# Performance work log

Hardware: AMD Instinct MI355X
Metric: run time of the kernel (lower is better)

Reference implementation:

```python
import jax, jax.numpy as jnp
import numpy as np

INPUT_SIZE = 3072
CORE_SIZE = 1024
OUTPUT_SIZE = 100
BATCH = 8192


def _ri(key, shape, lo, hi):
    # small-range int8 values (torch rand*scale cast to int8)
    return jax.random.randint(key, shape, lo, hi, dtype=jnp.int32).astype(jnp.int8)


def setup_inputs() -> dict:
    key = jax.random.key(0)
    ks = jax.random.split(key, 14)
    return {
        # learned int8 weights (nonzero after EQI.apply updates)
        "W_itoc": _ri(ks[0], (INPUT_SIZE, CORE_SIZE), -3, 4),
        "W_itoc_b": _ri(ks[1], (CORE_SIZE,), -3, 4),
        "W_ctoc": _ri(ks[2], (CORE_SIZE, CORE_SIZE), -3, 4),
        "W_ctoc_b": _ri(ks[3], (CORE_SIZE,), -3, 4),
        "W_ctoo": _ri(ks[4], (CORE_SIZE, OUTPUT_SIZE), -3, 4),
        "W_ctoo_b": _ri(ks[5], (OUTPUT_SIZE,), -3, 4),
        # epsilon perturbations: EPSILON_SCALE=2 -> values in {-1,0,1}
        "e_itoc": _ri(ks[6], (INPUT_SIZE, CORE_SIZE), -2, 2),
        "e_itoc_b": _ri(ks[7], (CORE_SIZE,), -2, 2),
        "e_ctoc": _ri(ks[8], (CORE_SIZE, CORE_SIZE), -2, 2),
        "e_ctoc_b": _ri(ks[9], (CORE_SIZE,), -2, 2),
        "e_ctoo": _ri(ks[10], (CORE_SIZE, OUTPUT_SIZE), -2, 2),
        "e_ctoo_b": _ri(ks[11], (OUTPUT_SIZE,), -2, 2),
        # forward activations
        "inputs": _ri(ks[12], (BATCH, INPUT_SIZE), -4, 5),
        "hiddens": _ri(ks[13], (BATCH, CORE_SIZE), -4, 5),
    }


def _addmm_i8(x, w, b):
    # int8 addmm with wraparound semantics: accumulate in int32, cast back
    # to int8 (truncation == mod-256, matching torch int8 arithmetic).
    acc = jnp.matmul(x.astype(jnp.int32), w.astype(jnp.int32)) + b.astype(jnp.int32)
    return acc.astype(jnp.int8)


def reference(W_itoc, W_itoc_b, W_ctoc, W_ctoc_b, W_ctoo, W_ctoo_b,
              e_itoc, e_itoc_b, e_ctoc, e_ctoc_b, e_ctoo, e_ctoo_b,
              inputs, hiddens):
    # layer 1: inputs -> core (weight = W + epsilon, elementwise int8 add)
    i2c = _addmm_i8(inputs, W_itoc + e_itoc, W_itoc_b + e_itoc_b)      # [B, CORE]
    # layer 2: (hiddens + projected inputs) -> core
    h2 = _addmm_i8(hiddens + i2c, W_ctoc + e_ctoc, W_ctoc_b + e_ctoc_b)  # [B, CORE]
    # layer 3: core -> output
    out = _addmm_i8(h2, W_ctoo + e_ctoo, W_ctoo_b + e_ctoo_b)          # [B, OUT]
    return (h2, out)
```

## Files before the change

kernel.cpp:

```cpp
#include <hip/hip_runtime.h>

typedef int v4i  __attribute__((ext_vector_type(4)));
typedef int v16i __attribute__((ext_vector_type(16)));

__device__ __forceinline__ int pack4i(int a, int b, int c, int d) {
  return (a & 255) | ((b & 255) << 8) | ((c & 255) << 16) | ((d & 255) << 24);
}
__device__ __forceinline__ int badd4(int a, int b) {
  return ((a & 0x7f7f7f7f) + (b & 0x7f7f7f7f)) ^ ((a ^ b) & 0x80808080);
}

#define MFMA_I8(a, b, c) __builtin_amdgcn_mfma_i32_32x32x32_i8(a, b, c, 0, 0, 0)
#define WAITV(N) asm volatile("s_waitcnt vmcnt(" #N ")" ::: "memory")
#define BARX do { asm volatile("s_waitcnt lgkmcnt(0)" ::: "memory"); \
                  __builtin_amdgcn_s_barrier(); } while (0)

__device__ void pack_tile(const int* __restrict__ W, const int* __restrict__ E,
                          char* __restrict__ Bt, int K, int N,
                          int nx, int ky, char* lin) {
  const int t = threadIdx.x;
  const int n0 = nx * 64, k0 = ky * 256;
  {
    const int c  = t & 15;
    const int kq = t >> 4;
    const int ng = n0 + c * 4;
    #pragma unroll 4
    for (int s = 0; s < 16; ++s) {
      const int k = s * 16 + kq;
      const long grow = (long)(k0 + k) * N;
      int a0, a1, a2, a3;
      if (ng + 3 < N) {
        int4 wv = *(const int4*)(W + grow + ng);
        int4 ev = *(const int4*)(E + grow + ng);
        a0 = wv.x + ev.x; a1 = wv.y + ev.y; a2 = wv.z + ev.z; a3 = wv.w + ev.w;
      } else {
        a0 = (ng + 0 < N) ? W[grow + ng + 0] + E[grow + ng + 0] : 0;
        a1 = (ng + 1 < N) ? W[grow + ng + 1] + E[grow + ng + 1] : 0;
        a2 = (ng + 2 < N) ? W[grow + ng + 2] + E[grow + ng + 2] : 0;
        a3 = (ng + 3 < N) ? W[grow + ng + 3] + E[grow + ng + 3] : 0;
      }
      *(int*)(lin + k * 68 + c * 4) = pack4i(a0, a1, a2, a3);
    }
  }
  __syncthreads();
  {
    const int n = t & 63, kq = t >> 6;
    char* dst = Bt + (long)(n0 + n) * K + k0 + (kq << 6);
    int outv[16];
    #pragma unroll
    for (int g = 0; g < 16; ++g) {
      const int k = (kq << 6) + (g << 2);
      outv[g] = pack4i(lin[(k + 0) * 68 + n], lin[(k + 1) * 68 + n],
                       lin[(k + 2) * 68 + n], lin[(k + 3) * 68 + n]);
    }
    #pragma unroll
    for (int g = 0; g < 4; ++g)
      *(int4*)(dst + (g << 4)) =
          make_int4(outv[g * 4], outv[g * 4 + 1], outv[g * 4 + 2], outv[g * 4 + 3]);
  }
}

__global__ __launch_bounds__(256) void pack_weights_kernel(
    const int* W1, const int* E1, char* Bt1,
    const int* W2, const int* E2, char* Bt2,
    const int* W3, const int* E3, char* Bt3,
    const int* b1, const int* eb1, int* bs1,
    const int* b2, const int* eb2, int* bs2,
    const int* b3, const int* eb3, int* bs3) {
  __shared__ __align__(16) char smem[17408];
  const int bid = blockIdx.x;
  if (bid < 192) {
    pack_tile(W1, E1, Bt1, 3072, 1024, bid % 16, bid / 16, smem);
  } else if (bid < 256) {
    const int l = bid - 192;
    pack_tile(W2, E2, Bt2, 1024, 1024, l % 16, l / 16, smem);
  } else if (bid < 264) {
    const int l = bid - 256;
    pack_tile(W3, E3, Bt3, 1024, 100, l & 1, l >> 1, smem);
  } else {
    const int t = threadIdx.x;
    for (int i = t; i < 1024; i += 256) {
      bs1[i] = b1[i] + eb1[i];
      bs2[i] = b2[i] + eb2[i];
    }
    for (int i = t; i < 128; i += 256)
      bs3[i] = (i < 100) ? (b3[i] + eb3[i]) : 0;
  }
}

__global__ __launch_bounds__(256, 2) void gemm1_kernel(
    const int* __restrict__ X, const char* __restrict__ Btg,
    const int* __restrict__ bsum, const int* __restrict__ H,
    char* __restrict__ A8out) {
  constexpr int K = 3072, KIT = 48;
  __shared__ __align__(16) char smem[61440];
  const int t = threadIdx.x;
  const int bid = blockIdx.x;
  const int mt = bid & 63, nt = bid >> 6;
  const long m0 = (long)mt << 7;
  const int n0 = nt << 7;

  const int lane = t & 63, w = t >> 6;
  const int lc = lane & 31, hg = lane >> 5;
  const int wm = w >> 1, wn = w & 1;

  v16i acc[2][2] = {};

  const int ar = t >> 4, ac = t & 15;
  const int* Xbase = X + (m0 + ar) * (long)K + ac * 4;
  const int awo = ar * 80 + ac * 4;
  const int r = t >> 2, q = t & 3;
  const char* Br0 = Btg + (long)(n0 + r) * K + q * 16;
  const char* Br1 = Br0 + (long)64 * K;
  const int bwo = 10240 + r * 80 + q * 16;

  const int fa = (wm * 64 + lc) * 80;
  const int fb = 10240 + (wn * 64 + lc) * 80;

  int4 xA[8], yA[8], xB0, xB1, yB0, yB1;

  auto ISSUEX = [&](int kt) {
    const int ko = kt * 64;
    #pragma unroll
    for (int j = 0; j < 8; ++j)
      xA[j] = *(const int4*)(Xbase + (long)j * 16 * K + ko);
    xB0 = *(const int4*)(Br0 + ko);
    xB1 = *(const int4*)(Br1 + ko);
  };
  auto ISSUEY = [&](int kt) {
    const int ko = kt * 64;
    #pragma unroll
    for (int j = 0; j < 8; ++j)
      yA[j] = *(const int4*)(Xbase + (long)j * 16 * K + ko);
    yB0 = *(const int4*)(Br0 + ko);
    yB1 = *(const int4*)(Br1 + ko);
  };
  auto WRITEX = [&](int st) {
    char* base = smem + st * 20480;
    #pragma unroll
    for (int j = 0; j < 8; ++j)
      *(int*)(base + awo + j * 16 * 80) =
          pack4i(xA[j].x, xA[j].y, xA[j].z, xA[j].w);
    *(int4*)(base + bwo)           = xB0;
    *(int4*)(base + bwo + 64 * 80) = xB1;
  };
  auto WRITEY = [&](int st) {
    char* base = smem + st * 20480;
    #pragma unroll
    for (int j = 0; j < 8; ++j)
      *(int*)(base + awo + j * 16 * 80) =
          pack4i(yA[j].x, yA[j].y, yA[j].z, yA[j].w);
    *(int4*)(base + bwo)           = yB0;
    *(int4*)(base + bwo + 64 * 80) = yB1;
  };
  auto MSTEP = [&](int st) {
    const char* base = smem + st * 20480;
    __builtin_amdgcn_s_setprio(1);
    #pragma unroll
    for (int ks = 0; ks < 2; ++ks) {
      const int sel = ks * 32 + hg * 16;
      v4i a0 = *(const v4i*)(base + fa + sel);
      v4i a1 = *(const v4i*)(base + fa + 32 * 80 + sel);
      v4i b0 = *(const v4i*)(base + fb + sel);
      v4i b1 = *(const v4i*)(base + fb + 32 * 80 + sel);
      acc[0][0] = MFMA_I8(a0, b0, acc[0][0]);
      acc[0][1] = MFMA_I8(a0, b1, acc[0][1]);
      acc[1][0] = MFMA_I8(a1, b0, acc[1][0]);
      acc[1][1] = MFMA_I8(a1, b1, acc[1][1]);
    }
    __builtin_amdgcn_s_setprio(0);
  };

  ISSUEX(0);
  ISSUEY(1);
  WAITV(10);
  WRITEX(0);
  BARX;
  for (int kt = 0; kt < KIT - 2; kt += 2) {
    ISSUEX(kt + 2);
    MSTEP(kt % 3);
    WAITV(10);
    WRITEY((kt + 1) % 3);
    BARX;
    ISSUEY(kt + 3);
    MSTEP((kt + 1) % 3);
    WAITV(10);
    WRITEX((kt + 2) % 3);
    BARX;
  }
  MSTEP((KIT - 2) % 3);
  WAITV(0);
  WRITEY((KIT - 1) % 3);
  BARX;
  MSTEP((KIT - 1) % 3);

  BARX;
  const int bsv0 = bsum[n0 + wn * 64 + lc];
  const int bsv1 = bsum[n0 + wn * 64 + 32 + lc];
  #pragma unroll
  for (int i = 0; i < 2; ++i) {
    #pragma unroll
    for (int j = 0; j < 2; ++j) {
      const int bv = j ? bsv1 : bsv0;
      const int col = wn * 64 + j * 32 + lc;
      #pragma unroll
      for (int rr = 0; rr < 16; ++rr) {
        const int row = wm * 64 + i * 32 + (hg << 2) + (rr & 3) + ((rr >> 2) << 3);
        smem[row * 136 + col] = (char)(acc[i][j][rr] + bv);
      }
    }
  }
  BARX;
  const char* srcp = smem + (t >> 1) * 136 + (t & 1) * 64;
  const long gco = (m0 + (t >> 1)) * 1024 + n0 + (t & 1) * 64;
  const int* hp = H + gco;
  #pragma unroll
  for (int g = 0; g < 4; ++g) {
    int4 s  = *(const int4*)(srcp + g * 16);
    int4 h0 = *(const int4*)(hp + g * 16);
    int4 h1 = *(const int4*)(hp + g * 16 + 4);
    int4 h2 = *(const int4*)(hp + g * 16 + 8);
    int4 h3 = *(const int4*)(hp + g * 16 + 12);
    s = make_int4(badd4(s.x, pack4i(h0.x, h0.y, h0.z, h0.w)),
                  badd4(s.y, pack4i(h1.x, h1.y, h1.z, h1.w)),
                  badd4(s.z, pack4i(h2.x, h2.y, h2.z, h2.w)),
                  badd4(s.w, pack4i(h3.x, h3.y, h3.z, h3.w)));
    *(int4*)(A8out + gco + g * 16) = s;
  }
}

__global__ __launch_bounds__(256, 2) void gemm2_kernel(
    const char* __restrict__ A, const char* __restrict__ Btg,
    const int* __restrict__ bsum, int* __restrict__ Iout) {
  constexpr int K = 1024, KIT = 16;
  __shared__ __align__(16) char smem[61440];
  const int t = threadIdx.x;
  const int bid = blockIdx.x;
  const int mt = bid & 63, nt = bid >> 6;
  const long m0 = (long)mt << 7;
  const int n0 = nt << 7;

  const int lane = t & 63, w = t >> 6;
  const int lc = lane & 31, hg = lane >> 5;
  const int wm = w >> 1, wn = w & 1;

  v16i acc[2][2] = {};

  const int r = t >> 2, q = t & 3;
  const char* Ar0 = A + (m0 + r) * (long)K + q * 16;
  const char* Ar1 = Ar0 + (long)64 * K;
  const char* Br0 = Btg + (long)(n0 + r) * K + q * 16;
  const char* Br1 = Br0 + (long)64 * K;
  const int awo = r * 80 + q * 16;
  const int bwo = 10240 + r * 80 + q * 16;

  const int fa = (wm * 64 + lc) * 80;
  const int fb = 10240 + (wn * 64 + lc) * 80;

  int4 xA0, xA1, xB0, xB1, yA0, yA1, yB0, yB1;

  auto ISSUEX = [&](int kt) {
    const int ko = kt * 64;
    xA0 = *(const int4*)(Ar0 + ko);
    xA1 = *(const int4*)(Ar1 + ko);
    xB0 = *(const int4*)(Br0 + ko);
    xB1 = *(const int4*)(Br1 + ko);
  };
  auto ISSUEY = [&](int kt) {
    const int ko = kt * 64;
    yA0 = *(const int4*)(Ar0 + ko);
    yA1 = *(const int4*)(Ar1 + ko);
    yB0 = *(const int4*)(Br0 + ko);
    yB1 = *(const int4*)(Br1 + ko);
  };
  auto WRITEX = [&](int st) {
    char* base = smem + st * 20480;
    *(int4*)(base + awo)           = xA0;
    *(int4*)(base + awo + 64 * 80) = xA1;
    *(int4*)(base + bwo)           = xB0;
    *(int4*)(base + bwo + 64 * 80) = xB1;
  };
  auto WRITEY = [&](int st) {
    char* base = smem + st * 20480;
    *(int4*)(base + awo)           = yA0;
    *(int4*)(base + awo + 64 * 80) = yA1;
    *(int4*)(base + bwo)           = yB0;
    *(int4*)(base + bwo + 64 * 80) = yB1;
  };
  auto MSTEP = [&](int st) {
    const char* base = smem + st * 20480;
    __builtin_amdgcn_s_setprio(1);
    #pragma unroll
    for (int ks = 0; ks < 2; ++ks) {
      const int sel = ks * 32 + hg * 16;
      v4i a0 = *(const v4i*)(base + fa + sel);
      v4i a1 = *(const v4i*)(base + fa + 32 * 80 + sel);
      v4i b0 = *(const v4i*)(base + fb + sel);
      v4i b1 = *(const v4i*)(base + fb + 32 * 80 + sel);
      acc[0][0] = MFMA_I8(a0, b0, acc[0][0]);
      acc[0][1] = MFMA_I8(a0, b1, acc[0][1]);
      acc[1][0] = MFMA_I8(a1, b0, acc[1][0]);
      acc[1][1] = MFMA_I8(a1, b1, acc[1][1]);
    }
    __builtin_amdgcn_s_setprio(0);
  };

  ISSUEX(0);
  ISSUEY(1);
  WAITV(4);
  WRITEX(0);
  BARX;
  for (int kt = 0; kt < KIT - 2; kt += 2) {
    ISSUEX(kt + 2);
    MSTEP(kt % 3);
    WAITV(4);
    WRITEY((kt + 1) % 3);
    BARX;
    ISSUEY(kt + 3);
    MSTEP((kt + 1) % 3);
    WAITV(4);
    WRITEX((kt + 2) % 3);
    BARX;
  }
  MSTEP((KIT - 2) % 3);
  WAITV(0);
  WRITEY((KIT - 1) % 3);
  BARX;
  MSTEP((KIT - 1) % 3);

  const int bsj0 = bsum[n0 + wn * 64 + lc];
  const int bsj1 = bsum[n0 + wn * 64 + 32 + lc];
  #pragma unroll
  for (int i = 0; i < 2; ++i) {
    #pragma unroll
    for (int j = 0; j < 2; ++j) {
      const int bv = j ? bsj1 : bsj0;
      const int col = n0 + wn * 64 + j * 32 + lc;
      #pragma unroll
      for (int rr = 0; rr < 16; ++rr) {
        const long row = m0 + wm * 64 + i * 32 + (hg << 2) + (rr & 3) + ((rr >> 2) << 3);
        Iout[row * 1024 + col] = (int)(signed char)(acc[i][j][rr] + bv);
      }
    }
  }
}

__global__ __launch_bounds__(256, 2) void gemm3_kernel(
    const int* __restrict__ h2, const char* __restrict__ Btg,
    const int* __restrict__ bsum, int* __restrict__ Iout) {
  __shared__ __align__(16) char smem[23040];
  const int t = threadIdx.x;
  const int m0 = blockIdx.x << 4;
  const int lane = t & 63, w = t >> 6;
  const int l16 = lane & 15, q = lane >> 4;
  v4i acc0 = {}, acc1 = {};

  const int am = t >> 4, ah = t & 15;
  const int* Arow = h2 + (long)(m0 + am) * 1024 + ah * 4;
  const int aoff = am * 80 + ah * 4;
  const int bm = t >> 1, bh = t & 1;
  const char* Brow = Btg + (long)bm * 1024 + bh * 32;
  const int boff = bm * 80 + bh * 32;

  const int abo  = l16 * 80 + q * 16;
  const int bbo0 = (w * 32 + l16) * 80 + q * 16;
  const int bbo1 = (w * 32 + 16 + l16) * 80 + q * 16;

  int4 ar, br0, br1;
  auto LOAD = [&](int kt) {
    const int kb = kt << 6;
    ar  = *(const int4*)(Arow + kb);
    br0 = *(const int4*)(Brow + kb);
    br1 = *(const int4*)(Brow + kb + 16);
  };
  auto STORE = [&](int stage) {
    char* base = smem + stage * 11520;
    *(int*)(base + aoff) = pack4i(ar.x, ar.y, ar.z, ar.w);
    *(int4*)(base + 1280 + boff)      = br0;
    *(int4*)(base + 1280 + boff + 16) = br1;
  };
  auto MFMA = [&](int stage) {
    const char* base = smem + stage * 11520;
    v4i a  = *(const v4i*)(base + abo);
    v4i b0 = *(const v4i*)(base + 1280 + bbo0);
    v4i b1 = *(const v4i*)(base + 1280 + bbo1);
    acc0 = __builtin_amdgcn_mfma_i32_16x16x64_i8(a, b0, acc0, 0, 0, 0);
    acc1 = __builtin_amdgcn_mfma_i32_16x16x64_i8(a, b1, acc1, 0, 0, 0);
  };

  LOAD(0); STORE(0); __syncthreads();
  for (int kt = 0; kt < 16; ++kt) {
    if (kt + 1 < 16) LOAD(kt + 1);
    MFMA(kt & 1);
    if (kt + 1 < 16) { STORE((kt + 1) & 1); __syncthreads(); }
  }

  const int c0 = w * 32 + l16;
  const int c1 = c0 + 16;
  if (c0 < 100) {
    const int b = bsum[c0];
    #pragma unroll
    for (int rr = 0; rr < 4; ++rr)
      Iout[(long)(m0 + q * 4 + rr) * 100 + c0] = (int)(signed char)(acc0[rr] + b);
  }
  if (c1 < 100) {
    const int b = bsum[c1];
    #pragma unroll
    for (int rr = 0; rr < 4; ++rr)
      Iout[(long)(m0 + q * 4 + rr) * 100 + c1] = (int)(signed char)(acc1[rr] + b);
  }
}

extern "C" void kernel_launch(void* const* d_in, const int* in_sizes, int n_in,
                              void* d_out, int out_size, void* d_ws, size_t ws_size,
                              hipStream_t stream) {
  (void)in_sizes; (void)n_in; (void)out_size; (void)ws_size;
  const int* W1  = (const int*)d_in[0];
  const int* b1  = (const int*)d_in[1];
  const int* W2  = (const int*)d_in[2];
  const int* b2  = (const int*)d_in[3];
  const int* W3  = (const int*)d_in[4];
  const int* b3  = (const int*)d_in[5];
  const int* E1  = (const int*)d_in[6];
  const int* eb1 = (const int*)d_in[7];
  const int* E2  = (const int*)d_in[8];
  const int* eb2 = (const int*)d_in[9];
  const int* E3  = (const int*)d_in[10];
  const int* eb3 = (const int*)d_in[11];
  const int* X   = (const int*)d_in[12];
  const int* H   = (const int*)d_in[13];
  int* out = (int*)d_out;

  char* ws  = (char*)d_ws;
  char* Bt1 = ws;
  char* Bt2 = Bt1 + 3145728;
  char* Bt3 = Bt2 + 1048576;
  int*  bs1 = (int*)(Bt3 + 131072);
  int*  bs2 = bs1 + 1024;
  int*  bs3 = bs2 + 1024;
  char* A2  = (char*)(bs3 + 128);

  pack_weights_kernel<<<dim3(265), dim3(256), 0, stream>>>(
      W1, E1, Bt1, W2, E2, Bt2, W3, E3, Bt3,
      b1, eb1, bs1, b2, eb2, bs2, b3, eb3, bs3);

  gemm1_kernel<<<dim3(512), dim3(256), 0, stream>>>(X, Bt1, bs1, H, A2);

  gemm2_kernel<<<dim3(512), dim3(256), 0, stream>>>(A2, Bt2, bs2, out);

  gemm3_kernel<<<dim3(512), dim3(256), 0, stream>>>(
      out, Bt3, bs3, out + 8388608);
}
```

Baseline: 295.9 us.

## Reshape GEMM1/GEMM2 tiles to 64x256 with double-buffered LDS pipeline

Changes the block tile of the first two int8 GEMMs from 128x128 to 64x256. The four waves now split only along N and share the A rows. The LDS pipeline moves from a triple buffer with one barrier per stage to a double buffer with an extra barrier before each write, and the tail iterations are folded into the loop with conditional issues. The goal is to cut wide int32 X loads per block and change how the staging buffer is used. The cost is more B traffic per tile and extra synchronisation per k-step.

```diff
diff --git a/kernel.cpp b/kernel.cpp
--- a/kernel.cpp
+++ b/kernel.cpp
@@ -93,68 +93,52 @@
     const int* __restrict__ bsum, const int* __restrict__ H,
     char* __restrict__ A8out) {
   constexpr int K = 3072, KIT = 48;
-  __shared__ __align__(16) char smem[61440];
+  __shared__ __align__(16) char smem[51200];
   const int t = threadIdx.x;
   const int bid = blockIdx.x;
-  const int mt = bid & 63, nt = bid >> 6;
-  const long m0 = (long)mt << 7;
-  const int n0 = nt << 7;
-
-  const int lane = t & 63, w = t >> 6;
+  const int mt = bid & 127, nt = bid >> 7;
+  const long m0 = (long)mt << 6;
+  const int n0 = nt << 8;
+
+  const int lane = t & 63, wn = t >> 6;
   const int lc = lane & 31, hg = lane >> 5;
-  const int wm = w >> 1, wn = w & 1;
 
   v16i acc[2][2] = {};
 
-  const int ar = t >> 4, ac = t & 15;
-  const int* Xbase = X + (m0 + ar) * (long)K + ac * 4;
-  const int awo = ar * 80 + ac * 4;
-  const int r = t >> 2, q = t & 3;
-  const char* Br0 = Btg + (long)(n0 + r) * K + q * 16;
-  const char* Br1 = Br0 + (long)64 * K;
-  const int bwo = 10240 + r * 80 + q * 16;
-
-  const int fa = (wm * 64 + lc) * 80;
-  const int fb = 10240 + (wn * 64 + lc) * 80;
-
-  int4 xA[8], yA[8], xB0, xB1, yB0, yB1;
-
-  auto ISSUEX = [&](int kt) {
-    const int ko = kt * 64;
-    #pragma unroll
-    for (int j = 0; j < 8; ++j)
-      xA[j] = *(const int4*)(Xbase + (long)j * 16 * K + ko);
-    xB0 = *(const int4*)(Br0 + ko);
-    xB1 = *(const int4*)(Br1 + ko);
-  };
-  auto ISSUEY = [&](int kt) {
-    const int ko = kt * 64;
-    #pragma unroll
-    for (int j = 0; j < 8; ++j)
-      yA[j] = *(const int4*)(Xbase + (long)j * 16 * K + ko);
-    yB0 = *(const int4*)(Br0 + ko);
-    yB1 = *(const int4*)(Br1 + ko);
-  };
-  auto WRITEX = [&](int st) {
-    char* base = smem + st * 20480;
-    #pragma unroll
-    for (int j = 0; j < 8; ++j)
-      *(int*)(base + awo + j * 16 * 80) =
-          pack4i(xA[j].x, xA[j].y, xA[j].z, xA[j].w);
-    *(int4*)(base + bwo)           = xB0;
-    *(int4*)(base + bwo + 64 * 80) = xB1;
-  };
-  auto WRITEY = [&](int st) {
-    char* base = smem + st * 20480;
-    #pragma unroll
-    for (int j = 0; j < 8; ++j)
-      *(int*)(base + awo + j * 16 * 80) =
-          pack4i(yA[j].x, yA[j].y, yA[j].z, yA[j].w);
-    *(int4*)(base + bwo)           = yB0;
-    *(int4*)(base + bwo + 64 * 80) = yB1;
-  };
+  const int ar16 = t >> 4, ac = t & 15;
+  const int* Xbase = X + (m0 + ar16) * (long)K + ac * 4;
+  const int awo = ar16 * 80 + ac * 4;
+  const int br4 = t >> 2, bc = t & 3;
+  const char* Bbase = Btg + (long)(n0 + br4) * K + bc * 16;
+  const int bwo = 5120 + br4 * 80 + bc * 16;
+
+  const int fa = lc * 80;
+  const int fb = 5120 + (wn * 64 + lc) * 80;
+
+  int4 xA[4], yA[4], xB[4], yB[4];
+
+#define G1_ISSUE(PA, PB, kt) do {                                   \
+    const int ko_ = (kt) * 64;                                      \
+    _Pragma("unroll")                                               \
+    for (int j = 0; j < 4; ++j)                                     \
+      PA[j] = *(const int4*)(Xbase + (long)j * 16 * K + ko_);       \
+    _Pragma("unroll")                                               \
+    for (int j = 0; j < 4; ++j)                                     \
+      PB[j] = *(const int4*)(Bbase + (long)j * 64 * K + ko_);       \
+  } while (0)
+#define G1_WRITE(PA, PB, st) do {                                   \
+    char* base_ = smem + (st) * 25600;                              \
+    _Pragma("unroll")                                               \
+    for (int j = 0; j < 4; ++j)                                     \
+      *(int*)(base_ + awo + j * 16 * 80) =                          \
+          pack4i(PA[j].x, PA[j].y, PA[j].z, PA[j].w);               \
+    _Pragma("unroll")                                               \
+    for (int j = 0; j < 4; ++j)                                     \
+      *(int4*)(base_ + bwo + j * 64 * 80) = PB[j];                  \
+  } while (0)
+
   auto MSTEP = [&](int st) {
-    const char* base = smem + st * 20480;
+    const char* base = smem + st * 25600;
     __builtin_amdgcn_s_setprio(1);
     #pragma unroll
     for (int ks = 0; ks < 2; ++ks) {
@@ -171,28 +155,28 @@
     __builtin_amdgcn_s_setprio(0);
   };
 
-  ISSUEX(0);
-  ISSUEY(1);
-  WAITV(10);
-  WRITEX(0);
+  G1_ISSUE(xA, xB, 0);
+  G1_ISSUE(yA, yB, 1);
+  WAITV(8);
+  G1_WRITE(xA, xB, 0);
   BARX;
-  for (int kt = 0; kt < KIT - 2; kt += 2) {
-    ISSUEX(kt + 2);
-    MSTEP(kt % 3);
-    WAITV(10);
-    WRITEY((kt + 1) % 3);
+
+  for (int kt = 0; kt < KIT; kt += 2) {
+    if (kt + 2 < KIT) G1_ISSUE(xA, xB, kt + 2);
+    MSTEP(kt & 1);
+    if (kt + 2 < KIT) WAITV(8); else WAITV(0);
     BARX;
-    ISSUEY(kt + 3);
-    MSTEP((kt + 1) % 3);
-    WAITV(10);
-    WRITEX((kt + 2) % 3);
+    G1_WRITE(yA, yB, (kt + 1) & 1);
     BARX;
-  }
-  MSTEP((KIT - 2) % 3);
-  WAITV(0);
-  WRITEY((KIT - 1) % 3);
-  BARX;
-  MSTEP((KIT - 1) % 3);
+    if (kt + 3 < KIT) G1_ISSUE(yA, yB, kt + 3);
+    MSTEP((kt + 1) & 1);
+    if (kt + 2 < KIT) {
+      if (kt + 3 < KIT) WAITV(8); else WAITV(0);
+      BARX;
+      G1_WRITE(xA, xB, (kt + 2) & 1);
+      BARX;
+    }
+  }
 
   BARX;
   const int bsv0 = bsum[n0 + wn * 64 + lc];
@@ -205,14 +189,14 @@
       const int col = wn * 64 + j * 32 + lc;
       #pragma unroll
       for (int rr = 0; rr < 16; ++rr) {
-        const int row = wm * 64 + i * 32 + (hg << 2) + (rr & 3) + ((rr >> 2) << 3);
-        smem[row * 136 + col] = (char)(acc[i][j][rr] + bv);
+        const int row = i * 32 + (hg << 2) + (rr & 3) + ((rr >> 2) << 3);
+        smem[row * 264 + col] = (char)(acc[i][j][rr] + bv);
       }
     }
   }
   BARX;
-  const char* srcp = smem + (t >> 1) * 136 + (t & 1) * 64;
-  const long gco = (m0 + (t >> 1)) * 1024 + n0 + (t & 1) * 64;
+  const char* srcp = smem + (t >> 2) * 264 + (t & 3) * 64;
+  const long gco = (m0 + (t >> 2)) * 1024 + n0 + (t & 3) * 64;
   const int* hp = H + gco;
   #pragma unroll
   for (int g = 0; g < 4; ++g) {
@@ -233,62 +217,46 @@
     const char* __restrict__ A, const char* __restrict__ Btg,
     const int* __restrict__ bsum, int* __restrict__ Iout) {
   constexpr int K = 1024, KIT = 16;
-  __shared__ __align__(16) char smem[61440];
+  __shared__ __align__(16) char smem[51200];
   const int t = threadIdx.x;
   const int bid = blockIdx.x;
-  const int mt = bid & 63, nt = bid >> 6;
-  const long m0 = (long)mt << 7;
-  const int n0 = nt << 7;
-
-  const int lane = t & 63, w = t >> 6;
+  const int mt = bid & 127, nt = bid >> 7;
+  const long m0 = (long)mt << 6;
+  const int n0 = nt << 8;
+
+  const int lane = t & 63, wn = t >> 6;
   const int lc = lane & 31, hg = lane >> 5;
-  const int wm = w >> 1, wn = w & 1;
 
   v16i acc[2][2] = {};
 
-  const int r = t >> 2, q = t & 3;
-  const char* Ar0 = A + (m0 + r) * (long)K + q * 16;
-  const char* Ar1 = Ar0 + (long)64 * K;
-  const char* Br0 = Btg + (long)(n0 + r) * K + q * 16;
-  const char* Br1 = Br0 + (long)64 * K;
-  const int awo = r * 80 + q * 16;
-  const int bwo = 10240 + r * 80 + q * 16;
-
-  const int fa = (wm * 64 + lc) * 80;
-  const int fb = 10240 + (wn * 64 + lc) * 80;
-
-  int4 xA0, xA1, xB0, xB1, yA0, yA1, yB0, yB1;
-
-  auto ISSUEX = [&](int kt) {
-    const int ko = kt * 64;
-    xA0 = *(const int4*)(Ar0 + ko);
-    xA1 = *(const int4*)(Ar1 + ko);
-    xB0 = *(const int4*)(Br0 + ko);
-    xB1 = *(const int4*)(Br1 + ko);
-  };
-  auto ISSUEY = [&](int kt) {
-    const int ko = kt * 64;
-    yA0 = *(const int4*)(Ar0 + ko);
-    yA1 = *(const int4*)(Ar1 + ko);
-    yB0 = *(const int4*)(Br0 + ko);
-    yB1 = *(const int4*)(Br1 + ko);
-  };
-  auto WRITEX = [&](int st) {
-    char* base = smem + st * 20480;
-    *(int4*)(base + awo)           = xA0;
-    *(int4*)(base + awo + 64 * 80) = xA1;
-    *(int4*)(base + bwo)           = xB0;
-    *(int4*)(base + bwo + 64 * 80) = xB1;
-  };
-  auto WRITEY = [&](int st) {
-    char* base = smem + st * 20480;
-    *(int4*)(base + awo)           = yA0;
-    *(int4*)(base + awo + 64 * 80) = yA1;
-    *(int4*)(base + bwo)           = yB0;
-    *(int4*)(base + bwo + 64 * 80) = yB1;
-  };
+  const int ar4 = t >> 2, ac4 = t & 3;
+  const char* Abase = A + (m0 + ar4) * (long)K + ac4 * 16;
+  const int awo = ar4 * 80 + ac4 * 16;
+  const char* Bbase = Btg + (long)(n0 + ar4) * K + ac4 * 16;
+  const int bwo = 5120 + ar4 * 80 + ac4 * 16;
+
+  const int fa = lc * 80;
+  const int fb = 5120 + (wn * 64 + lc) * 80;
+
+  int4 xA0, yA0, xB[4], yB[4];
+
+#define G2_ISSUE(PA, PB, kt) do {                                   \
+    const int ko_ = (kt) * 64;                                      \
+    PA = *(const int4*)(Abase + ko_);                               \
+    _Pragma("unroll")                                               \
+    for (int j = 0; j < 4; ++j)                                     \
+      PB[j] = *(const int4*)(Bbase + (long)j * 64 * K + ko_);       \
+  } while (0)
+#define G2_WRITE(PA, PB, st) do {                                   \
+    char* base_ = smem + (st) * 25600;                              \
+    *(int4*)(base_ + awo) = PA;                                     \
+    _Pragma("unroll")                                               \
+    for (int j = 0; j < 4; ++j)                                     \
+      *(int4*)(base_ + bwo + j * 64 * 80) = PB[j];                  \
+  } while (0)
+
   auto MSTEP = [&](int st) {
-    const char* base = smem + st * 20480;
+    const char* base = smem + st * 25600;
     __builtin_amdgcn_s_setprio(1);
     #pragma unroll
     for (int ks = 0; ks < 2; ++ks) {
@@ -305,28 +273,28 @@
     __builtin_amdgcn_s_setprio(0);
   };
 
-  ISSUEX(0);
-  ISSUEY(1);
-  WAITV(4);
-  WRITEX(0);
+  G2_ISSUE(xA0, xB, 0);
+  G2_ISSUE(yA0, yB, 1);
+  WAITV(5);
+  G2_WRITE(xA0, xB, 0);
   BARX;
-  for (int kt = 0; kt < KIT - 2; kt += 2) {
-    ISSUEX(kt + 2);
-    MSTEP(kt % 3);
-    WAITV(4);
-    WRITEY((kt + 1) % 3);
+
+  for (int kt = 0; kt < KIT; kt += 2) {
+    if (kt + 2 < KIT) G2_ISSUE(xA0, xB, kt + 2);
+    MSTEP(kt & 1);
+    if (kt + 2 < KIT) WAITV(5); else WAITV(0);
     BARX;
-    ISSUEY(kt + 3);
-    MSTEP((kt + 1) % 3);
-    WAITV(4);
-    WRITEX((kt + 2) % 3);
+    G2_WRITE(yA0, yB, (kt + 1) & 1);
     BARX;
-  }
-  MSTEP((KIT - 2) % 3);
-  WAITV(0);
-  WRITEY((KIT - 1) % 3);
-  BARX;
-  MSTEP((KIT - 1) % 3);
+    if (kt + 3 < KIT) G2_ISSUE(yA0, yB, kt + 3);
+    MSTEP((kt + 1) & 1);
+    if (kt + 2 < KIT) {
+      if (kt + 3 < KIT) WAITV(5); else WAITV(0);
+      BARX;
+      G2_WRITE(xA0, xB, (kt + 2) & 1);
+      BARX;
+    }
+  }
 
   const int bsj0 = bsum[n0 + wn * 64 + lc];
   const int bsj1 = bsum[n0 + wn * 64 + 32 + lc];
@@ -338,7 +306,7 @@
       const int col = n0 + wn * 64 + j * 32 + lc;
       #pragma unroll
       for (int rr = 0; rr < 16; ++rr) {
-        const long row = m0 + wm * 64 + i * 32 + (hg << 2) + (rr & 3) + ((rr >> 2) << 3);
+        const long row = m0 + i * 32 + (hg << 2) + (rr & 3) + ((rr >> 2) << 3);
         Iout[row * 1024 + col] = (int)(signed char)(acc[i][j][rr] + bv);
       }
     }
```

Measured after the change: 462.6 us. +56.4%, slower.

## Pre-pack int32 inputs to int8 buffer before gemm1

Applied to the files above, without the earlier changes.

Adds blocks to the packing kernel that convert the int32-stored input activations to packed int8 in the output buffer. gemm1 then loads 16-byte int8 rows for A like it does for B, instead of reading 4x wider int32 data every time each N-tile revisits the rows. This cuts gemm1 global traffic and packing ALU work inside the loop. The cost is an extra full pass over X (read 100MB int32, write 25MB) in the pre-pass, and the scratch buffer is the output buffer, which gemm2 overwrites later.

```diff
diff --git a/kernel.cpp b/kernel.cpp
--- a/kernel.cpp
+++ b/kernel.cpp
@@ -60,13 +60,14 @@
   }
 }
 
-__global__ __launch_bounds__(256) void pack_weights_kernel(
+__global__ __launch_bounds__(256) void pack_all_kernel(
     const int* W1, const int* E1, char* Bt1,
     const int* W2, const int* E2, char* Bt2,
     const int* W3, const int* E3, char* Bt3,
     const int* b1, const int* eb1, int* bs1,
     const int* b2, const int* eb2, int* bs2,
-    const int* b3, const int* eb3, int* bs3) {
+    const int* b3, const int* eb3, int* bs3,
+    const int* X, char* X8) {
   __shared__ __align__(16) char smem[17408];
   const int bid = blockIdx.x;
   if (bid < 192) {
@@ -77,7 +78,7 @@
   } else if (bid < 264) {
     const int l = bid - 256;
     pack_tile(W3, E3, Bt3, 1024, 100, l & 1, l >> 1, smem);
-  } else {
+  } else if (bid == 264) {
     const int t = threadIdx.x;
     for (int i = t; i < 1024; i += 256) {
       bs1[i] = b1[i] + eb1[i];
@@ -85,11 +86,26 @@
     }
     for (int i = t; i < 128; i += 256)
       bs3[i] = (i < 100) ? (b3[i] + eb3[i]) : 0;
+  } else {
+    const int t = threadIdx.x;
+    const long base = (long)(bid - 265) * 32768;
+    #pragma unroll 2
+    for (int it = 0; it < 8; ++it) {
+      const long o = base + it * 4096 + t * 4;
+      int4 a = *(const int4*)(X + o);
+      int4 b = *(const int4*)(X + o + 1024);
+      int4 c = *(const int4*)(X + o + 2048);
+      int4 d = *(const int4*)(X + o + 3072);
+      *(int*)(X8 + o)        = pack4i(a.x, a.y, a.z, a.w);
+      *(int*)(X8 + o + 1024) = pack4i(b.x, b.y, b.z, b.w);
+      *(int*)(X8 + o + 2048) = pack4i(c.x, c.y, c.z, c.w);
+      *(int*)(X8 + o + 3072) = pack4i(d.x, d.y, d.z, d.w);
+    }
   }
 }
 
 __global__ __launch_bounds__(256, 2) void gemm1_kernel(
-    const int* __restrict__ X, const char* __restrict__ Btg,
+    const char* __restrict__ A, const char* __restrict__ Btg,
     const int* __restrict__ bsum, const int* __restrict__ H,
     char* __restrict__ A8out) {
   constexpr int K = 3072, KIT = 48;
@@ -106,50 +122,44 @@
 
   v16i acc[2][2] = {};
 
-  const int ar = t >> 4, ac = t & 15;
-  const int* Xbase = X + (m0 + ar) * (long)K + ac * 4;
-  const int awo = ar * 80 + ac * 4;
   const int r = t >> 2, q = t & 3;
+  const char* Ar0 = A + (m0 + r) * (long)K + q * 16;
+  const char* Ar1 = Ar0 + (long)64 * K;
   const char* Br0 = Btg + (long)(n0 + r) * K + q * 16;
   const char* Br1 = Br0 + (long)64 * K;
+  const int awo = r * 80 + q * 16;
   const int bwo = 10240 + r * 80 + q * 16;
 
   const int fa = (wm * 64 + lc) * 80;
   const int fb = 10240 + (wn * 64 + lc) * 80;
 
-  int4 xA[8], yA[8], xB0, xB1, yB0, yB1;
+  int4 xA0, xA1, xB0, xB1, yA0, yA1, yB0, yB1;
 
   auto ISSUEX = [&](int kt) {
     const int ko = kt * 64;
-    #pragma unroll
-    for (int j = 0; j < 8; ++j)
-      xA[j] = *(const int4*)(Xbase + (long)j * 16 * K + ko);
+    xA0 = *(const int4*)(Ar0 + ko);
+    xA1 = *(const int4*)(Ar1 + ko);
     xB0 = *(const int4*)(Br0 + ko);
     xB1 = *(const int4*)(Br1 + ko);
   };
   auto ISSUEY = [&](int kt) {
     const int ko = kt * 64;
-    #pragma unroll
-    for (int j = 0; j < 8; ++j)
-      yA[j] = *(const int4*)(Xbase + (long)j * 16 * K + ko);
+    yA0 = *(const int4*)(Ar0 + ko);
+    yA1 = *(const int4*)(Ar1 + ko);
     yB0 = *(const int4*)(Br0 + ko);
     yB1 = *(const int4*)(Br1 + ko);
   };
   auto WRITEX = [&](int st) {
     char* base = smem + st * 20480;
-    #pragma unroll
-    for (int j = 0; j < 8; ++j)
-      *(int*)(base + awo + j * 16 * 80) =
-          pack4i(xA[j].x, xA[j].y, xA[j].z, xA[j].w);
+    *(int4*)(base + awo)           = xA0;
+    *(int4*)(base + awo + 64 * 80) = xA1;
     *(int4*)(base + bwo)           = xB0;
     *(int4*)(base + bwo + 64 * 80) = xB1;
   };
   auto WRITEY = [&](int st) {
     char* base = smem + st * 20480;
-    #pragma unroll
-    for (int j = 0; j < 8; ++j)
-      *(int*)(base + awo + j * 16 * 80) =
-          pack4i(yA[j].x, yA[j].y, yA[j].z, yA[j].w);
+    *(int4*)(base + awo)           = yA0;
+    *(int4*)(base + awo + 64 * 80) = yA1;
     *(int4*)(base + bwo)           = yB0;
     *(int4*)(base + bwo + 64 * 80) = yB1;
   };
@@ -173,18 +183,18 @@
 
   ISSUEX(0);
   ISSUEY(1);
-  WAITV(10);
+  WAITV(4);
   WRITEX(0);
   BARX;
   for (int kt = 0; kt < KIT - 2; kt += 2) {
     ISSUEX(kt + 2);
     MSTEP(kt % 3);
-    WAITV(10);
+    WAITV(4);
     WRITEY((kt + 1) % 3);
     BARX;
     ISSUEY(kt + 3);
     MSTEP((kt + 1) % 3);
-    WAITV(10);
+    WAITV(4);
     WRITEX((kt + 2) % 3);
     BARX;
   }
@@ -439,12 +449,13 @@
   int*  bs2 = bs1 + 1024;
   int*  bs3 = bs2 + 1024;
   char* A2  = (char*)(bs3 + 128);
-
-  pack_weights_kernel<<<dim3(265), dim3(256), 0, stream>>>(
+  char* X8  = (char*)d_out;
+
+  pack_all_kernel<<<dim3(1033), dim3(256), 0, stream>>>(
       W1, E1, Bt1, W2, E2, Bt2, W3, E3, Bt3,
-      b1, eb1, bs1, b2, eb2, bs2, b3, eb3, bs3);
-
-  gemm1_kernel<<<dim3(512), dim3(256), 0, stream>>>(X, Bt1, bs1, H, A2);
+      b1, eb1, bs1, b2, eb2, bs2, b3, eb3, bs3, X, X8);
+
+  gemm1_kernel<<<dim3(512), dim3(256), 0, stream>>>(X8, Bt1, bs1, H, A2);
 
   gemm2_kernel<<<dim3(512), dim3(256), 0, stream>>>(A2, Bt2, bs2, out);
 
```

New measurement: 292.2 us. No clear change (-1.2%).

## Pre-pack int32 inputs to int8 and widen gemm1 tile to 128x256

Applied to the files above, without the earlier changes.

Adds a separate kernel that converts the int32 input activations to packed int8, staging them in the output buffer, so gemm1 loads one quarter of the bytes for A. gemm1 now uses a 128x256 output tile with 2x4 MFMA accumulators per wave and half as many blocks, which raises reuse of each A fragment. The triple-buffered LDS ring becomes a double buffer of larger stages. In exchange there is an extra launch and a full int32 read plus int8 write of X, more accumulator registers, and only 256 blocks, which may underfill the device.

```diff
diff --git a/kernel.cpp b/kernel.cpp
--- a/kernel.cpp
+++ b/kernel.cpp
@@ -88,8 +88,34 @@
   }
 }
 
+__global__ __launch_bounds__(256) void pack_copy_kernel(
+    const int* __restrict__ X, char* __restrict__ X8) {
+  const int t = threadIdx.x;
+  const long base = (long)blockIdx.x * 32768;
+  #pragma unroll
+  for (int it = 0; it < 4; ++it) {
+    const long o = base + it * 8192 + t * 4;
+    int4 a0 = *(const int4*)(X + o);
+    int4 a1 = *(const int4*)(X + o + 1024);
+    int4 a2 = *(const int4*)(X + o + 2048);
+    int4 a3 = *(const int4*)(X + o + 3072);
+    int4 a4 = *(const int4*)(X + o + 4096);
+    int4 a5 = *(const int4*)(X + o + 5120);
+    int4 a6 = *(const int4*)(X + o + 6144);
+    int4 a7 = *(const int4*)(X + o + 7168);
+    *(int*)(X8 + o)        = pack4i(a0.x, a0.y, a0.z, a0.w);
+    *(int*)(X8 + o + 1024) = pack4i(a1.x, a1.y, a1.z, a1.w);
+    *(int*)(X8 + o + 2048) = pack4i(a2.x, a2.y, a2.z, a2.w);
+    *(int*)(X8 + o + 3072) = pack4i(a3.x, a3.y, a3.z, a3.w);
+    *(int*)(X8 + o + 4096) = pack4i(a4.x, a4.y, a4.z, a4.w);
+    *(int*)(X8 + o + 5120) = pack4i(a5.x, a5.y, a5.z, a5.w);
+    *(int*)(X8 + o + 6144) = pack4i(a6.x, a6.y, a6.z, a6.w);
+    *(int*)(X8 + o + 7168) = pack4i(a7.x, a7.y, a7.z, a7.w);
+  }
+}
+
 __global__ __launch_bounds__(256, 2) void gemm1_kernel(
-    const int* __restrict__ X, const char* __restrict__ Btg,
+    const char* __restrict__ A, const char* __restrict__ Btg,
     const int* __restrict__ bsum, const int* __restrict__ H,
     char* __restrict__ A8out) {
   constexpr int K = 3072, KIT = 48;
@@ -98,124 +124,126 @@
   const int bid = blockIdx.x;
   const int mt = bid & 63, nt = bid >> 6;
   const long m0 = (long)mt << 7;
-  const int n0 = nt << 7;
+  const int n0 = nt << 8;
 
   const int lane = t & 63, w = t >> 6;
   const int lc = lane & 31, hg = lane >> 5;
   const int wm = w >> 1, wn = w & 1;
 
-  v16i acc[2][2] = {};
-
-  const int ar = t >> 4, ac = t & 15;
-  const int* Xbase = X + (m0 + ar) * (long)K + ac * 4;
-  const int awo = ar * 80 + ac * 4;
+  v16i acc[2][4] = {};
+
   const int r = t >> 2, q = t & 3;
-  const char* Br0 = Btg + (long)(n0 + r) * K + q * 16;
-  const char* Br1 = Br0 + (long)64 * K;
+  const char* Ar0 = A + (m0 + r) * (long)K + q * 16;
+  const char* Ar1 = Ar0 + (long)64 * K;
+  const char* Bb  = Btg + (long)(n0 + r) * K + q * 16;
+  const int awo = r * 80 + q * 16;
   const int bwo = 10240 + r * 80 + q * 16;
 
-  const int fa = (wm * 64 + lc) * 80;
-  const int fb = 10240 + (wn * 64 + lc) * 80;
-
-  int4 xA[8], yA[8], xB0, xB1, yB0, yB1;
+  const int fa  = (wm * 64 + lc) * 80;
+  const int fbb = 10240 + (wn * 128 + lc) * 80;
+
+  int4 xA0, xA1, xB0, xB1, xB2, xB3;
+  int4 yA0, yA1, yB0, yB1, yB2, yB3;
 
   auto ISSUEX = [&](int kt) {
     const int ko = kt * 64;
-    #pragma unroll
-    for (int j = 0; j < 8; ++j)
-      xA[j] = *(const int4*)(Xbase + (long)j * 16 * K + ko);
-    xB0 = *(const int4*)(Br0 + ko);
-    xB1 = *(const int4*)(Br1 + ko);
+    xA0 = *(const int4*)(Ar0 + ko);
+    xA1 = *(const int4*)(Ar1 + ko);
+    xB0 = *(const int4*)(Bb + ko);
+    xB1 = *(const int4*)(Bb + (long)64 * K + ko);
+    xB2 = *(const int4*)(Bb + (long)128 * K + ko);
+    xB3 = *(const int4*)(Bb + (long)192 * K + ko);
   };
   auto ISSUEY = [&](int kt) {
     const int ko = kt * 64;
-    #pragma unroll
-    for (int j = 0; j < 8; ++j)
-      yA[j] = *(const int4*)(Xbase + (long)j * 16 * K + ko);
-    yB0 = *(const int4*)(Br0 + ko);
-    yB1 = *(const int4*)(Br1 + ko);
+    yA0 = *(const int4*)(Ar0 + ko);
+    yA1 = *(const int4*)(Ar1 + ko);
+    yB0 = *(const int4*)(Bb + ko);
+    yB1 = *(const int4*)(Bb + (long)64 * K + ko);
+    yB2 = *(const int4*)(Bb + (long)128 * K + ko);
+    yB3 = *(const int4*)(Bb + (long)192 * K + ko);
   };
   auto WRITEX = [&](int st) {
-    char* base = smem + st * 20480;
-    #pragma unroll
-    for (int j = 0; j < 8; ++j)
-      *(int*)(base + awo + j * 16 * 80) =
-          pack4i(xA[j].x, xA[j].y, xA[j].z, xA[j].w);
-    *(int4*)(base + bwo)           = xB0;
-    *(int4*)(base + bwo + 64 * 80) = xB1;
+    char* base = smem + st * 30720;
+    *(int4*)(base + awo)            = xA0;
+    *(int4*)(base + awo + 64 * 80)  = xA1;
+    *(int4*)(base + bwo)            = xB0;
+    *(int4*)(base + bwo + 64 * 80)  = xB1;
+    *(int4*)(base + bwo + 128 * 80) = xB2;
+    *(int4*)(base + bwo + 192 * 80) = xB3;
   };
   auto WRITEY = [&](int st) {
-    char* base = smem + st * 20480;
-    #pragma unroll
-    for (int j = 0; j < 8; ++j)
-      *(int*)(base + awo + j * 16 * 80) =
-          pack4i(yA[j].x, yA[j].y, yA[j].z, yA[j].w);
-    *(int4*)(base + bwo)           = yB0;
-    *(int4*)(base + bwo + 64 * 80) = yB1;
+    char* base = smem + st * 30720;
+    *(int4*)(base + awo)            = yA0;
+    *(int4*)(base + awo + 64 * 80)  = yA1;
+    *(int4*)(base + bwo)            = yB0;
+    *(int4*)(base + bwo + 64 * 80)  = yB1;
+    *(int4*)(base + bwo + 128 * 80) = yB2;
+    *(int4*)(base + bwo + 192 * 80) = yB3;
   };
   auto MSTEP = [&](int st) {
-    const char* base = smem + st * 20480;
+    const char* base = smem + st * 30720;
     __builtin_amdgcn_s_setprio(1);
     #pragma unroll
     for (int ks = 0; ks < 2; ++ks) {
       const int sel = ks * 32 + hg * 16;
       v4i a0 = *(const v4i*)(base + fa + sel);
       v4i a1 = *(const v4i*)(base + fa + 32 * 80 + sel);
-      v4i b0 = *(const v4i*)(base + fb + sel);
-      v4i b1 = *(const v4i*)(base + fb + 32 * 80 + sel);
-      acc[0][0] = MFMA_I8(a0, b0, acc[0][0]);
-      acc[0][1] = MFMA_I8(a0, b1, acc[0][1]);
-      acc[1][0] = MFMA_I8(a1, b0, acc[1][0]);
-      acc[1][1] = MFMA_I8(a1, b1, acc[1][1]);
+      #pragma unroll
+      for (int j = 0; j < 4; ++j) {
+        v4i b = *(const v4i*)(base + fbb + j * 32 * 80 + sel);
+        acc[0][j] = MFMA_I8(a0, b, acc[0][j]);
+        acc[1][j] = MFMA_I8(a1, b, acc[1][j]);
+      }
     }
     __builtin_amdgcn_s_setprio(0);
   };
 
   ISSUEX(0);
   ISSUEY(1);
-  WAITV(10);
+  WAITV(6);
   WRITEX(0);
   BARX;
   for (int kt = 0; kt < KIT - 2; kt += 2) {
     ISSUEX(kt + 2);
-    MSTEP(kt % 3);
-    WAITV(10);
-    WRITEY((kt + 1) % 3);
+    MSTEP(0);
+    WAITV(6);
+    WRITEY(1);
     BARX;
     ISSUEY(kt + 3);
-    MSTEP((kt + 1) % 3);
-    WAITV(10);
-    WRITEX((kt + 2) % 3);
+    MSTEP(1);
+    WAITV(6);
+    WRITEX(0);
     BARX;
   }
-  MSTEP((KIT - 2) % 3);
+  MSTEP(0);
   WAITV(0);
-  WRITEY((KIT - 1) % 3);
-  BARX;
-  MSTEP((KIT - 1) % 3);
-
-  BARX;
-  const int bsv0 = bsum[n0 + wn * 64 + lc];
-  const int bsv1 = bsum[n0 + wn * 64 + 32 + lc];
+  WRITEY(1);
+  BARX;
+  MSTEP(1);
+
+  BARX;
+  int bsv[4];
+  #pragma unroll
+  for (int j = 0; j < 4; ++j) bsv[j] = bsum[n0 + wn * 128 + j * 32 + lc];
   #pragma unroll
   for (int i = 0; i < 2; ++i) {
     #pragma unroll
-    for (int j = 0; j < 2; ++j) {
-      const int bv = j ? bsv1 : bsv0;
-      const int col = wn * 64 + j * 32 + lc;
+    for (int j = 0; j < 4; ++j) {
+      const int col = wn * 128 + j * 32 + lc;
       #pragma unroll
       for (int rr = 0; rr < 16; ++rr) {
         const int row = wm * 64 + i * 32 + (hg << 2) + (rr & 3) + ((rr >> 2) << 3);
-        smem[row * 136 + col] = (char)(acc[i][j][rr] + bv);
+        smem[row * 264 + col] = (char)(acc[i][j][rr] + bsv[j]);
       }
     }
   }
   BARX;
-  const char* srcp = smem + (t >> 1) * 136 + (t & 1) * 64;
-  const long gco = (m0 + (t >> 1)) * 1024 + n0 + (t & 1) * 64;
+  const char* srcp = smem + (t >> 1) * 264 + (t & 1) * 128;
+  const long gco = (m0 + (t >> 1)) * 1024 + n0 + (t & 1) * 128;
   const int* hp = H + gco;
   #pragma unroll
-  for (int g = 0; g < 4; ++g) {
+  for (int g = 0; g < 8; ++g) {
     int4 s  = *(const int4*)(srcp + g * 16);
     int4 h0 = *(const int4*)(hp + g * 16);
     int4 h1 = *(const int4*)(hp + g * 16 + 4);
@@ -439,12 +467,15 @@
   int*  bs2 = bs1 + 1024;
   int*  bs3 = bs2 + 1024;
   char* A2  = (char*)(bs3 + 128);
+  char* X8  = (char*)d_out;
 
   pack_weights_kernel<<<dim3(265), dim3(256), 0, stream>>>(
       W1, E1, Bt1, W2, E2, Bt2, W3, E3, Bt3,
       b1, eb1, bs1, b2, eb2, bs2, b3, eb3, bs3);
 
-  gemm1_kernel<<<dim3(512), dim3(256), 0, stream>>>(X, Bt1, bs1, H, A2);
+  pack_copy_kernel<<<dim3(768), dim3(256), 0, stream>>>(X, X8);
+
+  gemm1_kernel<<<dim3(256), dim3(256), 0, stream>>>(X8, Bt1, bs1, H, A2);
 
   gemm2_kernel<<<dim3(512), dim3(256), 0, stream>>>(A2, Bt2, bs2, out);
 
```

Result: no change. 296.7 us (+0.3%).
